# Optimization experiments

Measured on AMD Instinct MI355X. Metric: run time of the kernel, lower is better.

The kernel has to match this reference:

```python
import jax, jax.numpy as jnp
import numpy as np

N, D_IN, HEADS, D_HEAD = 16384, 512, 2, 512
D_CAT = HEADS * D_HEAD  # 1024
NEG_SLOPE = 0.2


def setup_inputs() -> dict:
    key = jax.random.key(0)
    ks = jax.random.split(key, 12)
    s = lambda d: 1.0 / np.sqrt(d)
    return {
        "x": jax.random.normal(ks[0], (N, D_IN), jnp.float32),
        "edge_index": jax.random.randint(ks[1], (2, 524288), 0, N, jnp.int64),
        "W": jax.random.normal(ks[2], (D_IN, D_CAT), jnp.float32) * s(D_IN),
        "att_src": jax.random.normal(ks[3], (HEADS, D_HEAD), jnp.float32) * s(D_HEAD),
        "att_dst": jax.random.normal(ks[4], (HEADS, D_HEAD), jnp.float32) * s(D_HEAD),
        "bias": jnp.zeros((D_CAT,), jnp.float32),
        "Wa": jax.random.normal(ks[5], (D_CAT, 128), jnp.float32) * s(D_CAT),
        "ba": jnp.zeros((128,), jnp.float32),
        "W1": jax.random.normal(ks[6], (128, 64), jnp.float32) * s(128),
        "b1": jnp.zeros((64,), jnp.float32),
        "W2": jax.random.normal(ks[7], (64, 3), jnp.float32) * s(64),
        "b2": jnp.zeros((3,), jnp.float32),
    }


def _gat_mlp(x, edge_index, W, att_src, att_dst, bias, Wa, ba, W1, b1, W2, b2):
    n = x.shape[0]
    # add self-loops (PyG GATConv default)
    loop = jnp.arange(n, dtype=edge_index.dtype)
    src = jnp.concatenate([edge_index[0], loop])
    dst = jnp.concatenate([edge_index[1], loop])

    xh = (x @ W).reshape(n, HEADS, D_HEAD)           # [N,H,C]
    a_src = jnp.einsum('nhc,hc->nh', xh, att_src)    # [N,H]
    a_dst = jnp.einsum('nhc,hc->nh', xh, att_dst)

    logits = jax.nn.leaky_relu(a_src[src] + a_dst[dst], NEG_SLOPE)  # [E,H]
    # segment softmax over incoming edges of each destination node
    m = jax.ops.segment_max(logits, dst, num_segments=n)
    e = jnp.exp(logits - m[dst])
    z = jax.ops.segment_sum(e, dst, num_segments=n)
    alpha = e / jnp.maximum(z[dst], 1e-16)           # [E,H]

    msg = xh[src] * alpha[:, :, None]                # [E,H,C]
    out = jax.ops.segment_sum(msg, dst, num_segments=n)  # [N,H,C]
    h = out.reshape(n, D_CAT) + bias

    h = jax.nn.relu(h)                # dropout is identity in eval
    h = jax.nn.relu(h @ Wa + ba)
    h = jax.nn.relu(h @ W1 + b1)
    h = h @ W2 + b2                   # [N,3]

    # cdist p=2
    sq = jnp.sum(h * h, axis=-1)
    d2 = sq[:, None] + sq[None, :] - 2.0 * (h @ h.T)
    d2 = jnp.maximum(d2, 0.0)
    safe = jnp.where(d2 > 0, d2, 1.0)
    return jnp.where(d2 > 0, jnp.sqrt(safe), 0.0)


def reference(x, edge_index, W, att_src, att_dst, bias, Wa, ba, W1, b1, W2, b2):
    return _gat_mlp(x, edge_index, W, att_src, att_dst, bias, Wa, ba, W1, b1, W2, b2)
```

## Files before the change

### kernel.cpp

```cpp
#include <hip/hip_runtime.h>

constexpr int N_NODES = 16384;
constexpr int DIN     = 512;
constexpr int DCAT    = 1024;
constexpr int NE      = 524288;
constexpr int ET      = NE + N_NODES;

__global__ __launch_bounds__(256) void detect_kernel(const int* __restrict__ ei,
                                                     int* __restrict__ flag) {
  int nz = 0;
  for (int i = threadIdx.x; i < 4096; i += 256) nz |= ei[2 * i + 1];
  if (nz) atomicOr(flag, 1);
}

__global__ __launch_bounds__(256) void count_kernel(const int* __restrict__ ei,
                                                    const int* __restrict__ flag,
                                                    int* __restrict__ cnt) {
  int e = blockIdx.x * 256 + threadIdx.x;
  if (e >= ET) return;
  int is64 = (*flag == 0);
  int dst;
  if (e < NE) {
    int di = NE + e;
    dst = ei[is64 ? 2 * di : di];
  } else {
    dst = e - NE;
  }
  atomicAdd(&cnt[dst], 1);
}

__global__ __launch_bounds__(1024) void scan_kernel(const int* __restrict__ cnt,
                                                    int* __restrict__ rowptr) {
  __shared__ int sums[1024];
  int tid = threadIdx.x;
  int local[16];
  int s = 0;
#pragma unroll
  for (int i = 0; i < 16; ++i) { local[i] = s; s += cnt[tid * 16 + i]; }
  sums[tid] = s;
  __syncthreads();
  for (int off = 1; off < 1024; off <<= 1) {
    int v = 0;
    if (tid >= off) v = sums[tid - off];
    __syncthreads();
    sums[tid] += v;
    __syncthreads();
  }
  int base = (tid == 0) ? 0 : sums[tid - 1];
#pragma unroll
  for (int i = 0; i < 16; ++i) rowptr[tid * 16 + i] = base + local[i];
  if (tid == 1023) rowptr[N_NODES] = sums[1023];
}

__global__ __launch_bounds__(256) void scatter_kernel(const int* __restrict__ ei,
                                                      const int* __restrict__ flag,
                                                      const int* __restrict__ rowptr,
                                                      int* __restrict__ cursor,
                                                      int* __restrict__ esrc) {
  int e = blockIdx.x * 256 + threadIdx.x;
  if (e >= ET) return;
  int is64 = (*flag == 0);
  int src, dst;
  if (e < NE) {
    src = ei[is64 ? 2 * e : e];
    int di = NE + e;
    dst = ei[is64 ? 2 * di : di];
  } else {
    src = dst = e - NE;
  }
  int pos = atomicAdd(&cursor[dst], 1);
  esrc[rowptr[dst] + pos] = src;
}

__global__ __launch_bounds__(256) void gemm1_kernel(const float* __restrict__ A,
                                                    const float* __restrict__ B,
                                                    float* __restrict__ C) {
  constexpr int BM = 128, BN = 128, BK = 8;
  __shared__ float As[BK][BM];
  __shared__ float Bs[BK][BN];
  int tid = threadIdx.x;
  int bm = blockIdx.y * BM;
  int bn = blockIdx.x * BN;
  int arow = tid >> 1, akq = (tid & 1) * 4;
  int brow = tid >> 5, bcol = (tid & 31) * 4;
  int tm = (tid >> 4) * 8;
  int tn = (tid & 15) * 8;
  float acc[8][8];
#pragma unroll
  for (int i = 0; i < 8; ++i)
#pragma unroll
    for (int j = 0; j < 8; ++j) acc[i][j] = 0.f;

  for (int k0 = 0; k0 < DIN; k0 += BK) {
    float4 a4 = *(const float4*)(A + (size_t)(bm + arow) * DIN + k0 + akq);
    As[akq + 0][arow] = a4.x;
    As[akq + 1][arow] = a4.y;
    As[akq + 2][arow] = a4.z;
    As[akq + 3][arow] = a4.w;
    *(float4*)(&Bs[brow][bcol]) =
        *(const float4*)(B + (size_t)(k0 + brow) * DCAT + bn + bcol);
    __syncthreads();
#pragma unroll
    for (int kk = 0; kk < BK; ++kk) {
      float a[8], b[8];
#pragma unroll
      for (int i = 0; i < 8; ++i) a[i] = As[kk][tm + i];
#pragma unroll
      for (int j = 0; j < 8; ++j) b[j] = Bs[kk][tn + j];
#pragma unroll
      for (int i = 0; i < 8; ++i)
#pragma unroll
        for (int j = 0; j < 8; ++j) acc[i][j] += a[i] * b[j];
    }
    __syncthreads();
  }
#pragma unroll
  for (int i = 0; i < 8; ++i)
#pragma unroll
    for (int j = 0; j < 8; j += 4) {
      float4 v = make_float4(acc[i][j], acc[i][j + 1], acc[i][j + 2], acc[i][j + 3]);
      *(float4*)(C + (size_t)(bm + tm + i) * DCAT + bn + tn + j) = v;
    }
}

__global__ __launch_bounds__(256) void avec_kernel(const float* __restrict__ xh,
                                                   const float* __restrict__ att_src,
                                                   const float* __restrict__ att_dst,
                                                   float* __restrict__ asrc,
                                                   float* __restrict__ adst) {
  int w = blockIdx.x * 4 + (threadIdx.x >> 6);
  int lane = threadIdx.x & 63;
  int n = w >> 1, h = w & 1;
  const float* row = xh + (size_t)n * DCAT + h * 512;
  const float* as = att_src + h * 512;
  const float* ad = att_dst + h * 512;
  float s1 = 0.f, s2 = 0.f;
  for (int c = lane; c < 512; c += 64) {
    float v = row[c];
    s1 += v * as[c];
    s2 += v * ad[c];
  }
  for (int off = 32; off > 0; off >>= 1) {
    s1 += __shfl_down(s1, off);
    s2 += __shfl_down(s2, off);
  }
  if (lane == 0) {
    asrc[n * 2 + h] = s1;
    adst[n * 2 + h] = s2;
  }
}

__global__ __launch_bounds__(256) void agg_kernel(const float* __restrict__ xh,
                                                  const float* __restrict__ asrc,
                                                  const float* __restrict__ adst,
                                                  const int* __restrict__ rowptr,
                                                  const int* __restrict__ esrc,
                                                  const float* __restrict__ bias,
                                                  float* __restrict__ hagg) {
  __shared__ float4 red[256];
  __shared__ int   sbuf[256];
  __shared__ float w0buf[256];
  __shared__ float w1buf[256];

  int dst = blockIdx.x;
  int tid = threadIdx.x;
  int start = rowptr[dst];
  int deg = rowptr[dst + 1] - start;
  float ad0 = adst[2 * dst], ad1 = adst[2 * dst + 1];

  float m0 = -1e30f, z0 = 0.f, m1 = -1e30f, z1 = 0.f;
  for (int i = tid; i < deg; i += 256) {
    int s = esrc[start + i];
    float l0 = asrc[2 * s] + ad0;     l0 = l0 > 0.f ? l0 : 0.2f * l0;
    float l1 = asrc[2 * s + 1] + ad1; l1 = l1 > 0.f ? l1 : 0.2f * l1;
    if (l0 > m0) { z0 = z0 * __expf(m0 - l0) + 1.f; m0 = l0; } else { z0 += __expf(l0 - m0); }
    if (l1 > m1) { z1 = z1 * __expf(m1 - l1) + 1.f; m1 = l1; } else { z1 += __expf(l1 - m1); }
  }
  red[tid] = make_float4(m0, z0, m1, z1);
  __syncthreads();
  for (int s = 128; s > 0; s >>= 1) {
    if (tid < s) {
      float4 a = red[tid], b = red[tid + s];
      float M0 = fmaxf(a.x, b.x);
      float Z0 = a.y * __expf(a.x - M0) + b.y * __expf(b.x - M0);
      float M1 = fmaxf(a.z, b.z);
      float Z1 = a.w * __expf(a.z - M1) + b.w * __expf(b.z - M1);
      red[tid] = make_float4(M0, Z0, M1, Z1);
    }
    __syncthreads();
  }
  float4 fin = red[0];
  float fm0 = fin.x, fm1 = fin.z;
  float rz0 = 1.f / fmaxf(fin.y, 1e-16f);
  float rz1 = 1.f / fmaxf(fin.w, 1e-16f);

  int c0 = tid * 4;
  bool head1 = (c0 >= 512);
  float4 acc = make_float4(0.f, 0.f, 0.f, 0.f);
  for (int ch = 0; ch < deg; ch += 256) {
    int cnt = min(256, deg - ch);
    __syncthreads();
    if (tid < cnt) {
      int s = esrc[start + ch + tid];
      sbuf[tid] = s;
      float l0 = asrc[2 * s] + ad0;     l0 = l0 > 0.f ? l0 : 0.2f * l0;
      float l1 = asrc[2 * s + 1] + ad1; l1 = l1 > 0.f ? l1 : 0.2f * l1;
      w0buf[tid] = __expf(l0 - fm0);
      w1buf[tid] = __expf(l1 - fm1);
    }
    __syncthreads();
    for (int j = 0; j < cnt; ++j) {
      float w = head1 ? w1buf[j] : w0buf[j];
      const float4 v = *(const float4*)(xh + (size_t)sbuf[j] * DCAT + c0);
      acc.x += w * v.x;
      acc.y += w * v.y;
      acc.z += w * v.z;
      acc.w += w * v.w;
    }
  }
  float rz = head1 ? rz1 : rz0;
  float4 b4 = *(const float4*)(bias + c0);
  float4 o;
  o.x = fmaxf(acc.x * rz + b4.x, 0.f);
  o.y = fmaxf(acc.y * rz + b4.y, 0.f);
  o.z = fmaxf(acc.z * rz + b4.z, 0.f);
  o.w = fmaxf(acc.w * rz + b4.w, 0.f);
  *(float4*)(hagg + (size_t)dst * DCAT + c0) = o;
}

__global__ __launch_bounds__(128) void mlp_kernel(const float* __restrict__ hagg,
                                                  const float* __restrict__ Wa,
                                                  const float* __restrict__ ba,
                                                  const float* __restrict__ W1,
                                                  const float* __restrict__ b1,
                                                  const float* __restrict__ W2,
                                                  const float* __restrict__ b2,
                                                  float* __restrict__ h3) {
  __shared__ float hrow[8][1024];
  __shared__ float h1[8][128];
  __shared__ float h2[8][64];
  int tid = threadIdx.x;
  int n0 = blockIdx.x * 8;

  const float4* srcv = (const float4*)(hagg + (size_t)n0 * DCAT);
  float4* dstv = (float4*)&hrow[0][0];
  for (int i = tid; i < 8 * 1024 / 4; i += 128) dstv[i] = srcv[i];
  __syncthreads();

  {
    float acc[8];
    float bj = ba[tid];
#pragma unroll
    for (int r = 0; r < 8; ++r) acc[r] = bj;
#pragma unroll 4
    for (int k = 0; k < 1024; ++k) {
      float w = Wa[k * 128 + tid];
#pragma unroll
      for (int r = 0; r < 8; ++r) acc[r] += hrow[r][k] * w;
    }
#pragma unroll
    for (int r = 0; r < 8; ++r) h1[r][tid] = fmaxf(acc[r], 0.f);
  }
  __syncthreads();

  {
    int j = tid & 63, half = tid >> 6;
    float a2[4];
    float bj = b1[j];
#pragma unroll
    for (int r = 0; r < 4; ++r) a2[r] = bj;
#pragma unroll 4
    for (int k = 0; k < 128; ++k) {
      float w = W1[k * 64 + j];
#pragma unroll
      for (int r = 0; r < 4; ++r) a2[r] += h1[half * 4 + r][k] * w;
    }
#pragma unroll
    for (int r = 0; r < 4; ++r) h2[half * 4 + r][j] = fmaxf(a2[r], 0.f);
  }
  __syncthreads();

  if (tid < 24) {
    int r = tid / 3, c = tid % 3;
    float s = b2[c];
#pragma unroll 4
    for (int k = 0; k < 64; ++k) s += h2[r][k] * W2[k * 3 + c];
    h3[(size_t)(n0 + r) * 3 + c] = s;
  }
}

__global__ __launch_bounds__(256) void cdist_kernel(const float* __restrict__ h3,
                                                    float* __restrict__ out) {
  int i = blockIdx.y;
  int j0 = blockIdx.x * 1024 + threadIdx.x * 4;
  float x0 = h3[(size_t)i * 3 + 0];
  float x1 = h3[(size_t)i * 3 + 1];
  float x2 = h3[(size_t)i * 3 + 2];
  const float* p = h3 + (size_t)j0 * 3;
  float4 q0 = ((const float4*)p)[0];
  float4 q1 = ((const float4*)p)[1];
  float4 q2 = ((const float4*)p)[2];
  auto dist = [&](float a, float b, float c) {
    float dx = x0 - a, dy = x1 - b, dz = x2 - c;
    return sqrtf(dx * dx + dy * dy + dz * dz);
  };
  float4 o;
  o.x = dist(q0.x, q0.y, q0.z);
  o.y = dist(q0.w, q1.x, q1.y);
  o.z = dist(q1.z, q1.w, q2.x);
  o.w = dist(q2.y, q2.z, q2.w);
  *(float4*)(out + (size_t)i * N_NODES + j0) = o;
}

extern "C" void kernel_launch(void* const* d_in, const int* in_sizes, int n_in,
                              void* d_out, int out_size, void* d_ws, size_t ws_size,
                              hipStream_t stream) {
  const float* x       = (const float*)d_in[0];
  const int*   ei      = (const int*)d_in[1];
  const float* W       = (const float*)d_in[2];
  const float* att_src = (const float*)d_in[3];
  const float* att_dst = (const float*)d_in[4];
  const float* bias    = (const float*)d_in[5];
  const float* Wa      = (const float*)d_in[6];
  const float* ba      = (const float*)d_in[7];
  const float* W1      = (const float*)d_in[8];
  const float* b1      = (const float*)d_in[9];
  const float* W2      = (const float*)d_in[10];
  const float* b2      = (const float*)d_in[11];
  float* out = (float*)d_out;

  float* xh   = (float*)d_ws;
  float* hagg = xh + (size_t)N_NODES * DCAT;
  float* asrc = hagg + (size_t)N_NODES * DCAT;
  float* adst = asrc + N_NODES * 2;
  float* h3   = adst + N_NODES * 2;
  int* rowptr = (int*)(h3 + (size_t)N_NODES * 3);
  int* cnt    = rowptr + 16388;
  int* cursor = cnt + N_NODES;
  int* flag   = cursor + N_NODES;
  int* esrc   = flag + 4;

  hipMemsetAsync(cnt, 0, (size_t)(N_NODES + N_NODES + 4) * sizeof(int), stream);

  detect_kernel<<<1, 256, 0, stream>>>(ei, flag);
  count_kernel<<<(ET + 255) / 256, 256, 0, stream>>>(ei, flag, cnt);
  scan_kernel<<<1, 1024, 0, stream>>>(cnt, rowptr);
  scatter_kernel<<<(ET + 255) / 256, 256, 0, stream>>>(ei, flag, rowptr, cursor, esrc);

  gemm1_kernel<<<dim3(DCAT / 128, N_NODES / 128), 256, 0, stream>>>(x, W, xh);
  avec_kernel<<<N_NODES * 2 / 4, 256, 0, stream>>>(xh, att_src, att_dst, asrc, adst);
  agg_kernel<<<N_NODES, 256, 0, stream>>>(xh, asrc, adst, rowptr, esrc, bias, hagg);
  mlp_kernel<<<N_NODES / 8, 128, 0, stream>>>(hagg, Wa, ba, W1, b1, W2, b2, h3);
  cdist_kernel<<<dim3(N_NODES / 1024, N_NODES), 256, 0, stream>>>(h3, out);
}
```

Before: 1.866 ms.

## Split MLP into register-tiled GEMM kernels and unroll aggregation gather loop

The fused per-8-row MLP kernel is replaced by two kernels. The first is a shared-memory tiled GEMM with 4x4 register blocking for hagg@Wa, which writes h1 to a new workspace buffer. The second is a tiled kernel for the 128->64->3 layers over 64-row blocks. Separately, the aggregation inner loop is unrolled by 4 so four independent row gathers can be in flight at once. This is meant to cut redundant Wa reads and raise FMA throughput, at the cost of an extra global round-trip for h1.

```diff
diff --git a/kernel.cpp b/kernel.cpp
--- a/kernel.cpp
+++ b/kernel.cpp
@@ -209,8 +209,22 @@
       w1buf[tid] = __expf(l1 - fm1);
     }
     __syncthreads();
-    for (int j = 0; j < cnt; ++j) {
-      float w = head1 ? w1buf[j] : w0buf[j];
+    const float* wbuf = head1 ? w1buf : w0buf;
+    int j = 0;
+    for (; j + 4 <= cnt; j += 4) {
+      int s0 = sbuf[j + 0], s1 = sbuf[j + 1], s2 = sbuf[j + 2], s3 = sbuf[j + 3];
+      float fw0 = wbuf[j + 0], fw1 = wbuf[j + 1], fw2 = wbuf[j + 2], fw3 = wbuf[j + 3];
+      float4 v0 = *(const float4*)(xh + (size_t)s0 * DCAT + c0);
+      float4 v1 = *(const float4*)(xh + (size_t)s1 * DCAT + c0);
+      float4 v2 = *(const float4*)(xh + (size_t)s2 * DCAT + c0);
+      float4 v3 = *(const float4*)(xh + (size_t)s3 * DCAT + c0);
+      acc.x += fw0 * v0.x; acc.y += fw0 * v0.y; acc.z += fw0 * v0.z; acc.w += fw0 * v0.w;
+      acc.x += fw1 * v1.x; acc.y += fw1 * v1.y; acc.z += fw1 * v1.z; acc.w += fw1 * v1.w;
+      acc.x += fw2 * v2.x; acc.y += fw2 * v2.y; acc.z += fw2 * v2.z; acc.w += fw2 * v2.w;
+      acc.x += fw3 * v3.x; acc.y += fw3 * v3.y; acc.z += fw3 * v3.z; acc.w += fw3 * v3.w;
+    }
+    for (; j < cnt; ++j) {
+      float w = wbuf[j];
       const float4 v = *(const float4*)(xh + (size_t)sbuf[j] * DCAT + c0);
       acc.x += w * v.x;
       acc.y += w * v.y;
@@ -228,63 +242,137 @@
   *(float4*)(hagg + (size_t)dst * DCAT + c0) = o;
 }
 
-__global__ __launch_bounds__(128) void mlp_kernel(const float* __restrict__ hagg,
-                                                  const float* __restrict__ Wa,
-                                                  const float* __restrict__ ba,
-                                                  const float* __restrict__ W1,
-                                                  const float* __restrict__ b1,
-                                                  const float* __restrict__ W2,
-                                                  const float* __restrict__ b2,
-                                                  float* __restrict__ h3) {
-  __shared__ float hrow[8][1024];
-  __shared__ float h1[8][128];
-  __shared__ float h2[8][64];
+__global__ __launch_bounds__(256) void mlpA_kernel(const float* __restrict__ hagg,
+                                                   const float* __restrict__ Wa,
+                                                   const float* __restrict__ ba,
+                                                   float* __restrict__ h1) {
+  constexpr int BM = 32, BK = 16;
+  __shared__ float Ast[BK][BM];
+  __shared__ float Bs[BK][128];
   int tid = threadIdx.x;
-  int n0 = blockIdx.x * 8;
-
-  const float4* srcv = (const float4*)(hagg + (size_t)n0 * DCAT);
-  float4* dstv = (float4*)&hrow[0][0];
-  for (int i = tid; i < 8 * 1024 / 4; i += 128) dstv[i] = srcv[i];
+  int bm = blockIdx.x * BM;
+  int rowg = tid >> 5;
+  int colg = tid & 31;
+  int tm = rowg * 4, tn = colg * 4;
+  float acc[4][4];
+#pragma unroll
+  for (int i = 0; i < 4; ++i)
+#pragma unroll
+    for (int j = 0; j < 4; ++j) acc[i][j] = 0.f;
+
+  int ar = tid >> 2;
+  int akq = (tid & 3) * 4;
+  for (int k0 = 0; k0 < DCAT; k0 += BK) {
+    if (tid < 128) {
+      float4 v = *(const float4*)(hagg + (size_t)(bm + ar) * DCAT + k0 + akq);
+      Ast[akq + 0][ar] = v.x;
+      Ast[akq + 1][ar] = v.y;
+      Ast[akq + 2][ar] = v.z;
+      Ast[akq + 3][ar] = v.w;
+    }
+    {
+      int r0 = tid >> 5, c0q = (tid & 31) * 4;
+      *(float4*)&Bs[r0][c0q] = *(const float4*)(Wa + (size_t)(k0 + r0) * 128 + c0q);
+      int r1 = r0 + 8;
+      *(float4*)&Bs[r1][c0q] = *(const float4*)(Wa + (size_t)(k0 + r1) * 128 + c0q);
+    }
+    __syncthreads();
+#pragma unroll
+    for (int kk = 0; kk < BK; ++kk) {
+      float4 a4 = *(const float4*)&Ast[kk][tm];
+      float4 b4 = *(const float4*)&Bs[kk][tn];
+      float av[4] = {a4.x, a4.y, a4.z, a4.w};
+      float bv[4] = {b4.x, b4.y, b4.z, b4.w};
+#pragma unroll
+      for (int i = 0; i < 4; ++i)
+#pragma unroll
+        for (int j = 0; j < 4; ++j) acc[i][j] += av[i] * bv[j];
+    }
+    __syncthreads();
+  }
+  float4 bb = *(const float4*)(ba + tn);
+  float bbv[4] = {bb.x, bb.y, bb.z, bb.w};
+#pragma unroll
+  for (int i = 0; i < 4; ++i) {
+    float4 o;
+    o.x = fmaxf(acc[i][0] + bbv[0], 0.f);
+    o.y = fmaxf(acc[i][1] + bbv[1], 0.f);
+    o.z = fmaxf(acc[i][2] + bbv[2], 0.f);
+    o.w = fmaxf(acc[i][3] + bbv[3], 0.f);
+    *(float4*)(h1 + (size_t)(bm + tm + i) * 128 + tn) = o;
+  }
+}
+
+__global__ __launch_bounds__(256) void mlpBC_kernel(const float* __restrict__ h1g,
+                                                    const float* __restrict__ W1,
+                                                    const float* __restrict__ b1,
+                                                    const float* __restrict__ W2,
+                                                    const float* __restrict__ b2,
+                                                    float* __restrict__ h3) {
+  __shared__ float sh1[64][132];
+  __shared__ float sW1[128][68];
+  __shared__ float sh2[64][68];
+  __shared__ float sW2[192];
+  int tid = threadIdx.x;
+  int n0 = blockIdx.x * 64;
+
+#pragma unroll
+  for (int q = 0; q < 8; ++q) {
+    int s = tid + q * 256;
+    int r = s >> 5, cq = (s & 31) * 4;
+    *(float4*)&sh1[r][cq] = *(const float4*)(h1g + (size_t)(n0 + r) * 128 + cq);
+  }
+#pragma unroll
+  for (int q = 0; q < 8; ++q) {
+    int s = tid + q * 256;
+    int r = s >> 4, cq = (s & 15) * 4;
+    *(float4*)&sW1[r][cq] = *(const float4*)(W1 + (size_t)r * 64 + cq);
+  }
+  if (tid < 192) sW2[tid] = W2[tid];
   __syncthreads();
 
   {
-    float acc[8];
-    float bj = ba[tid];
-#pragma unroll
-    for (int r = 0; r < 8; ++r) acc[r] = bj;
-#pragma unroll 4
-    for (int k = 0; k < 1024; ++k) {
-      float w = Wa[k * 128 + tid];
-#pragma unroll
-      for (int r = 0; r < 8; ++r) acc[r] += hrow[r][k] * w;
-    }
-#pragma unroll
-    for (int r = 0; r < 8; ++r) h1[r][tid] = fmaxf(acc[r], 0.f);
+    int rowg = tid >> 4, colg = tid & 15;
+    int rm = rowg * 4, cn = colg * 4;
+    float acc[4][4];
+#pragma unroll
+    for (int i = 0; i < 4; ++i)
+#pragma unroll
+      for (int j = 0; j < 4; ++j) acc[i][j] = 0.f;
+    for (int k0 = 0; k0 < 128; k0 += 4) {
+      float av[4][4], bv[4][4];
+#pragma unroll
+      for (int i = 0; i < 4; ++i) {
+        float4 a = *(const float4*)&sh1[rm + i][k0];
+        av[i][0] = a.x; av[i][1] = a.y; av[i][2] = a.z; av[i][3] = a.w;
+      }
+#pragma unroll
+      for (int kk = 0; kk < 4; ++kk) {
+        float4 b = *(const float4*)&sW1[k0 + kk][cn];
+        bv[kk][0] = b.x; bv[kk][1] = b.y; bv[kk][2] = b.z; bv[kk][3] = b.w;
+      }
+#pragma unroll
+      for (int i = 0; i < 4; ++i)
+#pragma unroll
+        for (int j = 0; j < 4; ++j)
+#pragma unroll
+          for (int kk = 0; kk < 4; ++kk) acc[i][j] += av[i][kk] * bv[kk][j];
+    }
+    float4 bb = *(const float4*)(b1 + cn);
+    float bbv[4] = {bb.x, bb.y, bb.z, bb.w};
+#pragma unroll
+    for (int i = 0; i < 4; ++i)
+#pragma unroll
+      for (int j = 0; j < 4; ++j)
+        sh2[rm + i][cn + j] = fmaxf(acc[i][j] + bbv[j], 0.f);
   }
   __syncthreads();
 
-  {
-    int j = tid & 63, half = tid >> 6;
-    float a2[4];
-    float bj = b1[j];
-#pragma unroll
-    for (int r = 0; r < 4; ++r) a2[r] = bj;
-#pragma unroll 4
-    for (int k = 0; k < 128; ++k) {
-      float w = W1[k * 64 + j];
-#pragma unroll
-      for (int r = 0; r < 4; ++r) a2[r] += h1[half * 4 + r][k] * w;
-    }
-#pragma unroll
-    for (int r = 0; r < 4; ++r) h2[half * 4 + r][j] = fmaxf(a2[r], 0.f);
-  }
-  __syncthreads();
-
-  if (tid < 24) {
+  if (tid < 192) {
     int r = tid / 3, c = tid % 3;
     float s = b2[c];
 #pragma unroll 4
-    for (int k = 0; k < 64; ++k) s += h2[r][k] * W2[k * 3 + c];
+    for (int k = 0; k < 64; ++k) s += sh2[r][k] * sW2[k * 3 + c];
     h3[(size_t)(n0 + r) * 3 + c] = s;
   }
 }
@@ -334,7 +422,8 @@
   float* asrc = hagg + (size_t)N_NODES * DCAT;
   float* adst = asrc + N_NODES * 2;
   float* h3   = adst + N_NODES * 2;
-  int* rowptr = (int*)(h3 + (size_t)N_NODES * 3);
+  float* h1   = h3 + (size_t)N_NODES * 3;
+  int* rowptr = (int*)(h1 + (size_t)N_NODES * 128);
   int* cnt    = rowptr + 16388;
   int* cursor = cnt + N_NODES;
   int* flag   = cursor + N_NODES;
@@ -350,6 +439,7 @@
   gemm1_kernel<<<dim3(DCAT / 128, N_NODES / 128), 256, 0, stream>>>(x, W, xh);
   avec_kernel<<<N_NODES * 2 / 4, 256, 0, stream>>>(xh, att_src, att_dst, asrc, adst);
   agg_kernel<<<N_NODES, 256, 0, stream>>>(xh, asrc, adst, rowptr, esrc, bias, hagg);
-  mlp_kernel<<<N_NODES / 8, 128, 0, stream>>>(hagg, Wa, ba, W1, b1, W2, b2, h3);
+  mlpA_kernel<<<N_NODES / 32, 256, 0, stream>>>(hagg, Wa, ba, h1);
+  mlpBC_kernel<<<N_NODES / 64, 256, 0, stream>>>(h1, W1, b1, W2, b2, h3);
   cdist_kernel<<<dim3(N_NODES / 1024, N_NODES), 256, 0, stream>>>(h3, out);
 }
```

Result: faster. 1.735 ms (-7.0%).
